# Kernel tuning notes

Hardware: AMD Instinct MI355X
Metric: run time of the kernel (lower is better)

## Reference

```python
import jax, jax.numpy as jnp
import numpy as np

B, V, E = 2, 50000, 400000
FIN, COND, HID, OUT, ENC, EDG = 128, 32, 256, 128, 64, 16
EPS = 1e-5


def setup_inputs() -> dict:
    key = jax.random.key(0)
    ks = jax.random.split(key, 24)
    rn = lambda k, shp, s=0.05: jax.random.normal(k, shp, jnp.float32) * s
    return {
        "x": jax.random.normal(ks[0], (B, V, FIN), jnp.float32),
        "cond_x": jax.random.normal(ks[1], (V, COND), jnp.float32),
        "edge_attr": jax.random.normal(ks[2], (E, EDG), jnp.float32),
        "t": jax.random.normal(ks[3], (B, ENC), jnp.float32),
        "edge_index": jax.random.randint(ks[4], (2, E), 0, V, dtype=jnp.int32),
        # GCNConv weights (in, hid) + bias; Linear weights (hid, out) + bias
        "w_c0": rn(ks[5], (FIN + COND, HID)), "b_c0": rn(ks[6], (HID,)),
        "w_l0": rn(ks[7], (HID, HID)), "b_l0": rn(ks[8], (HID,)),
        "w_c1": rn(ks[9], (HID, HID)), "b_c1": rn(ks[10], (HID,)),
        "w_l1": rn(ks[11], (HID, HID)), "b_l1": rn(ks[12], (HID,)),
        "w_c2": rn(ks[13], (HID, HID)), "b_c2": rn(ks[14], (HID,)),
        "w_l2": rn(ks[15], (HID, OUT)), "b_l2": rn(ks[16], (OUT,)),
        "gn_g": jnp.ones((HID,), jnp.float32), "gn_b": jnp.zeros((HID,), jnp.float32),
        "film_w": rn(ks[17], (ENC, 2 * HID)), "film_b": rn(ks[18], (2 * HID,)),
    }


def _gcn(h, src, dst, dinv, W, b):
    # GCNConv: symmetric-normalized aggregation with self loops, then +bias.
    hw = h @ W  # (B, V, H)
    coef = (dinv[src] * dinv[dst])[None, :, None]            # (1, E, 1)
    self_loop = hw * (dinv * dinv)[None, :, None]            # norm of (i,i) edge
    agg = self_loop.at[:, dst, :].add(hw[:, src, :] * coef)  # scatter-add over dst
    return agg + b


def _groupnorm1(h, gamma, beta):
    # nn.GroupNorm(1, C) applied to (B, C, V): normalize over (C, V) per sample.
    mu = h.mean(axis=(1, 2), keepdims=True)
    var = ((h - mu) ** 2).mean(axis=(1, 2), keepdims=True)
    return (h - mu) * jax.lax.rsqrt(var + EPS) * gamma + beta


def reference(x, cond_x, edge_attr, t, edge_index,
              w_c0, b_c0, w_l0, b_l0, w_c1, b_c1, w_l1, b_l1,
              w_c2, b_c2, w_l2, b_l2, gn_g, gn_b, film_w, film_b):
    src, dst = edge_index[0], edge_index[1]
    deg = jnp.ones((V,), jnp.float32).at[dst].add(1.0)  # 1 = self loop
    dinv = jax.lax.rsqrt(deg)

    x_skip = x
    cond = jnp.broadcast_to(cond_x[None], (x.shape[0], V, COND))
    h = jnp.concatenate([x, cond], axis=-1)  # (B, V, FIN+COND)

    # layer 0: feature dim != hidden -> no norm
    h = jax.nn.relu(_gcn(h, src, dst, dinv, w_c0, b_c0))
    h = jax.nn.relu(h @ w_l0 + b_l0)  # dropout p=0 -> identity

    # layer 1: GroupNorm(1, hidden) then conv/linear
    h = _groupnorm1(h, gn_g, gn_b)
    h = jax.nn.relu(_gcn(h, src, dst, dinv, w_c1, b_c1))
    h = jax.nn.relu(h @ w_l1 + b_l1)

    # final gconv + FiLM + relu + linear + residual
    h = _gcn(h, src, dst, dinv, w_c2, b_c2)
    gb = t @ film_w + film_b                 # (B, 2*HID)
    gamma, beta = gb[:, :HID], gb[:, HID:]
    h = h * gamma[:, None, :] + beta[:, None, :]
    h = jax.nn.relu(h)
    out = h @ w_l2 + b_l2 + x_skip
    return out
```

## Files before the change

### kernel.cpp

```cpp
#include <hip/hip_runtime.h>
#include <stdint.h>

typedef unsigned short u16;
typedef short bf16x8 __attribute__((ext_vector_type(8)));
typedef float f32x4 __attribute__((ext_vector_type(4)));

constexpr int B_ = 2, V_ = 50000, E_ = 400000;
constexpr int FIN_ = 128, COND_ = 32, HID_ = 256, OUT_ = 128, ENC_ = 64;
constexpr int M_ = B_ * V_;
constexpr int MP_ = M_ + 256;
constexpr int K0_ = FIN_ + COND_;
constexpr float EPS_ = 1e-5f;

#define DEV static __device__ __forceinline__

DEV float b2f(u16 u) { union { float f; uint32_t i; } x; x.i = ((uint32_t)u) << 16; return x.f; }
DEV u16 f2b(float f) {
  union { float f; uint32_t i; } x; x.f = f;
  uint32_t r = x.i + 0x7fffu + ((x.i >> 16) & 1u);
  return (u16)(r >> 16);
}
DEV uint32_t pk2(float a, float b) { return (uint32_t)f2b(a) | ((uint32_t)f2b(b) << 16); }

#define GLDS16(gp, lp) __builtin_amdgcn_global_load_lds( \
    (const __attribute__((address_space(1))) void*)(gp), \
    (__attribute__((address_space(3))) void*)(lp), 16, 0, 0)

__global__ void k_count(const int* __restrict__ dst, int* __restrict__ cnt) {
  int e = blockIdx.x * blockDim.x + threadIdx.x;
  if (e < E_) atomicAdd(&cnt[dst[e]], 1);
}

__global__ void k_dinv(const int* __restrict__ cnt, float* __restrict__ dinv) {
  int v = blockIdx.x * blockDim.x + threadIdx.x;
  if (v < V_) dinv[v] = rsqrtf(1.0f + (float)cnt[v]);
}

__global__ __launch_bounds__(1024) void k_scan1(const int* __restrict__ cnt,
                                                int* __restrict__ tmp, int* __restrict__ bsum) {
  __shared__ int s[1024];
  int tid = threadIdx.x;
  int i = blockIdx.x * 1024 + tid;
  int v = (i < V_) ? cnt[i] : 0;
  s[tid] = v;
  __syncthreads();
  for (int off = 1; off < 1024; off <<= 1) {
    int t = (tid >= off) ? s[tid - off] : 0;
    __syncthreads();
    s[tid] += t;
    __syncthreads();
  }
  if (i < V_) tmp[i] = s[tid];
  if (tid == 1023) bsum[blockIdx.x] = s[1023];
}

__global__ void k_scan2(int* __restrict__ bsum, int n) {
  if (threadIdx.x == 0) {
    int a = 0;
    for (int i = 0; i < n; ++i) { a += bsum[i]; bsum[i] = a; }
  }
}

__global__ void k_scan3(const int* __restrict__ cnt, const int* __restrict__ tmp,
                        const int* __restrict__ bsum, int* __restrict__ row_ptr,
                        int* __restrict__ cursor) {
  int i = blockIdx.x * blockDim.x + threadIdx.x;
  if (i >= V_) return;
  int blk = i >> 10;
  int offs = blk ? bsum[blk - 1] : 0;
  int incl = tmp[i] + offs;
  row_ptr[i + 1] = incl;
  cursor[i] = incl - cnt[i];
  if (i == 0) row_ptr[0] = 0;
}

__global__ void k_fill(const int* __restrict__ src, const int* __restrict__ dst,
                       const float* __restrict__ dinv,
                       int* __restrict__ cursor, int2* __restrict__ csr) {
  int e = blockIdx.x * blockDim.x + threadIdx.x;
  if (e < E_) {
    int s = src[e], d = dst[e];
    int p = atomicAdd(&cursor[d], 1);
    float cf = dinv[s] * dinv[d];
    csr[p] = make_int2(s, __float_as_int(cf));
  }
}

__global__ void k_film(const float* __restrict__ t, const float* __restrict__ fw,
                       const float* __restrict__ fb, float* __restrict__ gb) {
  int b = blockIdx.x; int j = threadIdx.x;
  float acc = fb[j];
  for (int k = 0; k < ENC_; ++k) acc += t[b * ENC_ + k] * fw[k * 512 + j];
  gb[b * 512 + j] = acc;
}

__global__ void k_wconv(const float* __restrict__ W, u16* __restrict__ WT, int K, int N) {
  int idx = blockIdx.x * blockDim.x + threadIdx.x;
  if (idx < K * N) {
    int k = idx / N, n = idx % N;
    WT[n * K + k] = f2b(W[idx]);
  }
}

__global__ void k_wconv_g(const float* __restrict__ W, const float* __restrict__ gng,
                          u16* __restrict__ WT, int K, int N) {
  int idx = blockIdx.x * blockDim.x + threadIdx.x;
  if (idx < K * N) {
    int k = idx / N, n = idx % N;
    WT[n * K + k] = f2b(W[idx] * gng[k]);
  }
}

__global__ void k_gnreduce(const float4* __restrict__ part, int nblk,
                           float* __restrict__ stats) {
  int tid = threadIdx.x;
  float s0 = 0.f, ss0 = 0.f, s1 = 0.f, ss1 = 0.f;
  for (int i = tid; i < nblk; i += 256) {
    float4 p = part[i];
    s0 += p.x; ss0 += p.y; s1 += p.z; ss1 += p.w;
  }
  __shared__ float red[4][4];
#pragma unroll
  for (int o = 32; o > 0; o >>= 1) {
    s0  += __shfl_down(s0, o, 64);
    ss0 += __shfl_down(ss0, o, 64);
    s1  += __shfl_down(s1, o, 64);
    ss1 += __shfl_down(ss1, o, 64);
  }
  int w = tid >> 6, ln = tid & 63;
  if (ln == 0) { red[w][0] = s0; red[w][1] = ss0; red[w][2] = s1; red[w][3] = ss1; }
  __syncthreads();
  if (tid == 0) {
    float S0 = red[0][0] + red[1][0] + red[2][0] + red[3][0];
    float SS0 = red[0][1] + red[1][1] + red[2][1] + red[3][1];
    float S1 = red[0][2] + red[1][2] + red[2][2] + red[3][2];
    float SS1 = red[0][3] + red[1][3] + red[2][3] + red[3][3];
    float n = (float)V_ * (float)HID_;
    float mu0 = S0 / n, var0 = SS0 / n - mu0 * mu0;
    float mu1 = S1 / n, var1 = SS1 / n - mu1 * mu1;
    stats[0] = mu0; stats[1] = rsqrtf(var0 + EPS_);
    stats[2] = mu1; stats[3] = rsqrtf(var1 + EPS_);
  }
}

__global__ void k_gnfold(const float* __restrict__ gng, const float* __restrict__ gnb,
                         const float* __restrict__ W, const float* __restrict__ stats,
                         float* __restrict__ kc) {
  int n = blockIdx.x, c = threadIdx.x;
  float wv = W[c * HID_ + n];
  float gw = gng[c] * wv, bw = gnb[c] * wv;
  __shared__ float sg[4], sb[4];
#pragma unroll
  for (int o = 32; o > 0; o >>= 1) {
    gw += __shfl_down(gw, o, 64);
    bw += __shfl_down(bw, o, 64);
  }
  int w = c >> 6, ln = c & 63;
  if (ln == 0) { sg[w] = gw; sb[w] = bw; }
  __syncthreads();
  if (c == 0) {
    float G = sg[0] + sg[1] + sg[2] + sg[3];
    float Bw = sb[0] + sb[1] + sb[2] + sb[3];
    for (int b = 0; b < B_; ++b)
      kc[b * HID_ + n] = Bw - stats[b * 2] * stats[b * 2 + 1] * G;
  }
}

__global__ void k_prep0(const float* __restrict__ x, const float* __restrict__ cond,
                        u16* __restrict__ A0) {
  int idx = blockIdx.x * blockDim.x + threadIdx.x;
  if (idx >= M_ * K0_ / 4) return;
  int e = idx * 4;
  int r = e / K0_, c = e % K0_;
  float4 v;
  if (c < FIN_) v = *(const float4*)&x[(size_t)r * FIN_ + c];
  else { int vv = r % V_; v = *(const float4*)&cond[(size_t)vv * COND_ + (c - FIN_)]; }
  uint2 o;
  o.x = pk2(v.x, v.y);
  o.y = pk2(v.z, v.w);
  *(uint2*)&A0[e] = o;
}

template<int MODE>
__global__ __launch_bounds__(256) void k_gather(
    const u16* __restrict__ hw, const float* __restrict__ dinv,
    const int* __restrict__ row_ptr, const int2* __restrict__ csr,
    const float* __restrict__ bias, const float* __restrict__ gb,
    u16* __restrict__ out)
{
  __shared__ f32x4 redA[3][2][32];
  __shared__ f32x4 redB[3][2][32];
  const int v   = blockIdx.x;
  const int tid = threadIdx.x;
  const int nb  = tid >> 6;
  const int b   = (tid >> 5) & 1;
  const int l   = tid & 31;
  const int c0  = l * 8;

  const float dv = dinv[v];
  const int beg = row_ptr[v], end = row_ptr[v + 1];

  float acc[8];
#pragma unroll
  for (int k = 0; k < 8; ++k) acc[k] = 0.f;

  int j = beg + nb;
  for (; j + 4 < end; j += 8) {
    int2 e0 = csr[j];
    int2 e1 = csr[j + 4];
    float cf0 = __int_as_float(e0.y);
    float cf1 = __int_as_float(e1.y);
    uint4 u0 = *(const uint4*)&hw[((size_t)b * V_ + e0.x) * HID_ + c0];
    uint4 u1 = *(const uint4*)&hw[((size_t)b * V_ + e1.x) * HID_ + c0];
    u16 a0[8]; *(uint4*)a0 = u0;
    u16 a1[8]; *(uint4*)a1 = u1;
#pragma unroll
    for (int k = 0; k < 8; ++k) acc[k] += b2f(a0[k]) * cf0;
#pragma unroll
    for (int k = 0; k < 8; ++k) acc[k] += b2f(a1[k]) * cf1;
  }
  if (j < end) {
    int2 e0 = csr[j];
    float cf0 = __int_as_float(e0.y);
    uint4 u0 = *(const uint4*)&hw[((size_t)b * V_ + e0.x) * HID_ + c0];
    u16 a0[8]; *(uint4*)a0 = u0;
#pragma unroll
    for (int k = 0; k < 8; ++k) acc[k] += b2f(a0[k]) * cf0;
  }

  if (nb > 0) {
    redA[nb - 1][b][l] = f32x4{acc[0], acc[1], acc[2], acc[3]};
    redB[nb - 1][b][l] = f32x4{acc[4], acc[5], acc[6], acc[7]};
  }
  __syncthreads();
  if (nb == 0) {
#pragma unroll
    for (int g = 0; g < 3; ++g) {
      f32x4 ra = redA[g][b][l], rb = redB[g][b][l];
      acc[0] += ra[0]; acc[1] += ra[1]; acc[2] += ra[2]; acc[3] += ra[3];
      acc[4] += rb[0]; acc[5] += rb[1]; acc[6] += rb[2]; acc[7] += rb[3];
    }
    float sl = dv * dv;
    uint4 u = *(const uint4*)&hw[((size_t)b * V_ + v) * HID_ + c0];
    u16 us[8]; *(uint4*)us = u;
#pragma unroll
    for (int k = 0; k < 8; ++k) {
      float a = acc[k] + b2f(us[k]) * sl + bias[c0 + k];
      if (MODE == 1) a = fmaxf(a, 0.f);
      if (MODE == 2) {
        a = a * gb[b * 512 + c0 + k] + gb[b * 512 + 256 + c0 + k];
        a = fmaxf(a, 0.f);
      }
      acc[k] = a;
    }
    uint4 o;
    o.x = pk2(acc[0], acc[1]);
    o.y = pk2(acc[2], acc[3]);
    o.z = pk2(acc[4], acc[5]);
    o.w = pk2(acc[6], acc[7]);
    *(uint4*)&out[((size_t)b * V_ + v) * HID_ + c0] = o;
  }
}

template<int EPI, int K, int N>
__global__ __launch_bounds__(256) void k_gemm_g(
    const u16* __restrict__ A, const u16* __restrict__ WT,
    const float* __restrict__ p0,
    const float* __restrict__ stats,
    const float* __restrict__ xres,
    float4* __restrict__ part,
    void* __restrict__ Out)
{
  constexpr int BM = 128, BN = 128, BK = 32;
  __shared__ alignas(16) u16 As[BM * BK];
  __shared__ alignas(16) u16 Bs[BN * BK];
  __shared__ float sred[4][4];
  const int tile_m = blockIdx.x * BM;
  const int n0 = blockIdx.y * BN;
  const int tid = threadIdx.x;
  const int wave = tid >> 6, lane = tid & 63;
  const int wm = (wave >> 1) * 64, wn = (wave & 1) * 64;
  const int lr = lane & 15, lkg = lane >> 4;
  const int phys = lkg ^ ((lr >> 1) & 3);

  f32x4 acc[4][4];
#pragma unroll
  for (int i = 0; i < 4; ++i)
#pragma unroll
    for (int jj = 0; jj < 4; ++jj) acc[i][jj] = {0.f, 0.f, 0.f, 0.f};

  for (int kb = 0; kb < K; kb += BK) {
#pragma unroll
    for (int it = 0; it < 2; ++it) {
      int c = tid + it * 256;
      int row = c >> 2;
      int sslot = (c & 3) ^ ((row >> 1) & 3);
      GLDS16(A + (size_t)(tile_m + row) * K + kb + sslot * 8,
             &As[(it * 256 + wave * 64) * 8]);
    }
#pragma unroll
    for (int it = 0; it < 2; ++it) {
      int c = tid + it * 256;
      int row = c >> 2;
      int sslot = (c & 3) ^ ((row >> 1) & 3);
      GLDS16(WT + (size_t)(n0 + row) * K + kb + sslot * 8,
             &Bs[(it * 256 + wave * 64) * 8]);
    }
    __syncthreads();
    bf16x8 af[4], bf[4];
#pragma unroll
    for (int fm = 0; fm < 4; ++fm) af[fm] = *(const bf16x8*)&As[(wm + fm * 16 + lr) * BK + phys * 8];
#pragma unroll
    for (int fn = 0; fn < 4; ++fn) bf[fn] = *(const bf16x8*)&Bs[(wn + fn * 16 + lr) * BK + phys * 8];
#pragma unroll
    for (int fm = 0; fm < 4; ++fm)
#pragma unroll
      for (int fn = 0; fn < 4; ++fn)
        acc[fm][fn] = __builtin_amdgcn_mfma_f32_16x16x32_bf16(bf[fn], af[fm], acc[fm][fn], 0, 0, 0);
    __syncthreads();
  }

  float s0 = 0.f, ss0 = 0.f, s1 = 0.f, ss1 = 0.f;
#pragma unroll
  for (int fm = 0; fm < 4; ++fm) {
    const int row = tile_m + wm + fm * 16 + lr;
    if (row >= M_) continue;
#pragma unroll
    for (int fn = 0; fn < 4; ++fn) {
      const int colb = n0 + wn + fn * 16 + lkg * 4;
      float v0 = acc[fm][fn][0], v1 = acc[fm][fn][1];
      float v2 = acc[fm][fn][2], v3 = acc[fm][fn][3];
      if (EPI == 1 || EPI == 4) {
        float4 bs = *(const float4*)&p0[colb];
        v0 = fmaxf(v0 + bs.x, 0.f); v1 = fmaxf(v1 + bs.y, 0.f);
        v2 = fmaxf(v2 + bs.z, 0.f); v3 = fmaxf(v3 + bs.w, 0.f);
      }
      if (EPI == 4) {
        if (row >= V_) { s1 += v0 + v1 + v2 + v3; ss1 += v0*v0 + v1*v1 + v2*v2 + v3*v3; }
        else           { s0 += v0 + v1 + v2 + v3; ss0 += v0*v0 + v1*v1 + v2*v2 + v3*v3; }
      }
      if (EPI == 3) {
        int bb = (row >= V_) ? 1 : 0;
        float rs = stats[bb * 2 + 1];
        float4 kcv = *(const float4*)&p0[bb * N + colb];
        v0 = v0 * rs + kcv.x; v1 = v1 * rs + kcv.y;
        v2 = v2 * rs + kcv.z; v3 = v3 * rs + kcv.w;
      }
      if (EPI == 2) {
        float4 bs = *(const float4*)&p0[colb];
        float4 xr = *(const float4*)&xres[(size_t)row * N + colb];
        float4 o;
        o.x = v0 + bs.x + xr.x; o.y = v1 + bs.y + xr.y;
        o.z = v2 + bs.z + xr.z; o.w = v3 + bs.w + xr.w;
        *(float4*)&((float*)Out)[(size_t)row * N + colb] = o;
      } else {
        uint2 o;
        o.x = pk2(v0, v1);
        o.y = pk2(v2, v3);
        *(uint2*)&((u16*)Out)[(size_t)row * N + colb] = o;
      }
    }
  }
  if (EPI == 4) {
#pragma unroll
    for (int o = 32; o > 0; o >>= 1) {
      s0  += __shfl_down(s0, o, 64);
      ss0 += __shfl_down(ss0, o, 64);
      s1  += __shfl_down(s1, o, 64);
      ss1 += __shfl_down(ss1, o, 64);
    }
    if (lane == 0) { sred[wave][0] = s0; sred[wave][1] = ss0; sred[wave][2] = s1; sred[wave][3] = ss1; }
    __syncthreads();
    if (tid == 0) {
      float4 p;
      p.x = sred[0][0] + sred[1][0] + sred[2][0] + sred[3][0];
      p.y = sred[0][1] + sred[1][1] + sred[2][1] + sred[3][1];
      p.z = sred[0][2] + sred[1][2] + sred[2][2] + sred[3][2];
      p.w = sred[0][3] + sred[1][3] + sred[2][3] + sred[3][3];
      part[blockIdx.y * gridDim.x + blockIdx.x] = p;
    }
  }
}

extern "C" void kernel_launch(void* const* d_in, const int* in_sizes, int n_in,
                              void* d_out, int out_size, void* d_ws, size_t ws_size,
                              hipStream_t stream) {
  (void)in_sizes; (void)n_in; (void)out_size; (void)ws_size;
  const float* x      = (const float*)d_in[0];
  const float* cond_x = (const float*)d_in[1];
  const float* t      = (const float*)d_in[3];
  const int*   ei     = (const int*)d_in[4];
  const float* w_c0 = (const float*)d_in[5];  const float* b_c0 = (const float*)d_in[6];
  const float* w_l0 = (const float*)d_in[7];  const float* b_l0 = (const float*)d_in[8];
  const float* w_c1 = (const float*)d_in[9];  const float* b_c1 = (const float*)d_in[10];
  const float* w_l1 = (const float*)d_in[11]; const float* b_l1 = (const float*)d_in[12];
  const float* w_c2 = (const float*)d_in[13]; const float* b_c2 = (const float*)d_in[14];
  const float* w_l2 = (const float*)d_in[15]; const float* b_l2 = (const float*)d_in[16];
  const float* gn_g = (const float*)d_in[17]; const float* gn_b = (const float*)d_in[18];
  const float* film_w = (const float*)d_in[19]; const float* film_b = (const float*)d_in[20];

  char* wsp = (char*)d_ws;
  size_t off = 0;
  auto alloc = [&](size_t bytes) -> char* {
    char* p = wsp + off; off += (bytes + 255) & ~(size_t)255; return p;
  };
  constexpr int GM = (M_ + 127) / 128;
  int*   cnt       = (int*)  alloc((size_t)V_ * 4);
  int*   row_ptr   = (int*)  alloc((size_t)(V_ + 1) * 4);
  int*   cursor    = (int*)  alloc((size_t)V_ * 4);
  int2*  csr       = (int2*) alloc((size_t)E_ * 8);
  int*   scan_tmp  = (int*)  alloc((size_t)V_ * 4);
  int*   scan_bsum = (int*)  alloc(64 * 4);
  float* dinv      = (float*)alloc((size_t)V_ * 4);
  float* stats     = (float*)alloc(16);
  float4* part     = (float4*)alloc((size_t)GM * 2 * 16);
  float* gb        = (float*)alloc(2 * 512 * 4);
  float* kc        = (float*)alloc(2 * HID_ * 4);
  u16* wc0T  = (u16*)alloc((size_t)256 * 160 * 2);
  u16* wl0T  = (u16*)alloc((size_t)256 * 256 * 2);
  u16* wc1Tg = (u16*)alloc((size_t)256 * 256 * 2);
  u16* wl1T  = (u16*)alloc((size_t)256 * 256 * 2);
  u16* wc2T  = (u16*)alloc((size_t)256 * 256 * 2);
  u16* wl2T  = (u16*)alloc((size_t)128 * 256 * 2);
  u16* A0    = (u16*)alloc((size_t)MP_ * K0_ * 2);
  u16* HW    = (u16*)alloc((size_t)MP_ * HID_ * 2);
  u16* HA    = (u16*)alloc((size_t)MP_ * HID_ * 2);
  u16* HB    = (u16*)alloc((size_t)MP_ * HID_ * 2);

  const int* srcI = ei;
  const int* dstI = ei + E_;

  hipMemsetAsync(cnt, 0, (size_t)V_ * 4, stream);

  constexpr int NBLK = (V_ + 1023) / 1024;
  k_count<<<dim3((E_ + 255) / 256), dim3(256), 0, stream>>>(dstI, cnt);
  k_dinv <<<dim3((V_ + 255) / 256), dim3(256), 0, stream>>>(cnt, dinv);
  k_scan1<<<dim3(NBLK), dim3(1024), 0, stream>>>(cnt, scan_tmp, scan_bsum);
  k_scan2<<<dim3(1), dim3(64), 0, stream>>>(scan_bsum, NBLK);
  k_scan3<<<dim3((V_ + 255) / 256), dim3(256), 0, stream>>>(cnt, scan_tmp, scan_bsum, row_ptr, cursor);
  k_fill <<<dim3((E_ + 255) / 256), dim3(256), 0, stream>>>(srcI, dstI, dinv, cursor, csr);
  k_film <<<dim3(2), dim3(512), 0, stream>>>(t, film_w, film_b, gb);

  k_wconv  <<<dim3((160 * 256 + 255) / 256), dim3(256), 0, stream>>>(w_c0, wc0T, 160, 256);
  k_wconv  <<<dim3((256 * 256 + 255) / 256), dim3(256), 0, stream>>>(w_l0, wl0T, 256, 256);
  k_wconv_g<<<dim3((256 * 256 + 255) / 256), dim3(256), 0, stream>>>(w_c1, gn_g, wc1Tg, 256, 256);
  k_wconv  <<<dim3((256 * 256 + 255) / 256), dim3(256), 0, stream>>>(w_l1, wl1T, 256, 256);
  k_wconv  <<<dim3((256 * 256 + 255) / 256), dim3(256), 0, stream>>>(w_c2, wc2T, 256, 256);
  k_wconv  <<<dim3((256 * 128 + 255) / 256), dim3(256), 0, stream>>>(w_l2, wl2T, 256, 128);

  k_prep0<<<dim3(M_ * K0_ / 4 / 256), dim3(256), 0, stream>>>(x, cond_x, A0);

  k_gemm_g<0, 160, 256><<<dim3(GM, 2), 256, 0, stream>>>(A0, wc0T, nullptr, nullptr, nullptr, nullptr, HW);
  k_gather<1><<<dim3(V_), 256, 0, stream>>>(HW, dinv, row_ptr, csr, b_c0, nullptr, HA);
  k_gemm_g<4, 256, 256><<<dim3(GM, 2), 256, 0, stream>>>(HA, wl0T, b_l0, nullptr, nullptr, part, HB);

  k_gnreduce<<<dim3(1), dim3(256), 0, stream>>>(part, GM * 2, stats);
  k_gnfold <<<dim3(256), dim3(256), 0, stream>>>(gn_g, gn_b, w_c1, stats, kc);

  k_gemm_g<3, 256, 256><<<dim3(GM, 2), 256, 0, stream>>>(HB, wc1Tg, kc, stats, nullptr, nullptr, HW);
  k_gather<1><<<dim3(V_), 256, 0, stream>>>(HW, dinv, row_ptr, csr, b_c1, nullptr, HA);
  k_gemm_g<1, 256, 256><<<dim3(GM, 2), 256, 0, stream>>>(HA, wl1T, b_l1, nullptr, nullptr, nullptr, HB);

  k_gemm_g<0, 256, 256><<<dim3(GM, 2), 256, 0, stream>>>(HB, wc2T, nullptr, nullptr, nullptr, nullptr, HW);
  k_gather<2><<<dim3(V_), 256, 0, stream>>>(HW, dinv, row_ptr, csr, b_c2, gb, HA);
  k_gemm_g<2, 256, 128><<<dim3(GM, 1), 256, 0, stream>>>(HA, wl2T, b_l2, nullptr, x, nullptr, (void*)d_out);
}
```

Measured before the change: 525.2 us.

## Aggregate before GEMM and fuse each conv GEMM with following linear GEMM

Reorders each GCN layer to aggregate over neighbours first (A·H then W), so layer 0 gathers the 160-wide input instead of the 256-wide projection. Each conv GEMM is then fused with the following linear GEMM in one kernel that keeps the 64x256 intermediate tile in LDS, which removes one full write and read of the hidden activations per layer. The GroupNorm fold is moved after aggregation by using a per-node rowsum of edge coefficients. In exchange the fused kernel uses smaller 64-row tiles and needs a large LDS footprint, which may lower occupancy, and the gather kernel idles some lanes when the width is 160.

```diff
diff --git a/kernel.cpp b/kernel.cpp
--- a/kernel.cpp
+++ b/kernel.cpp
@@ -84,6 +84,17 @@
     float cf = dinv[s] * dinv[d];
     csr[p] = make_int2(s, __float_as_int(cf));
   }
+}
+
+__global__ void k_rowsum(const float* __restrict__ dinv, const int* __restrict__ row_ptr,
+                         const int2* __restrict__ csr, float* __restrict__ rowsum) {
+  int v = blockIdx.x * blockDim.x + threadIdx.x;
+  if (v >= V_) return;
+  float dv = dinv[v];
+  float s = dv * dv;
+  int e = row_ptr[v + 1];
+  for (int j = row_ptr[v]; j < e; ++j) s += __int_as_float(csr[j].y);
+  rowsum[v] = s;
 }
 
 __global__ void k_film(const float* __restrict__ t, const float* __restrict__ fw,
@@ -181,11 +192,10 @@
   *(uint2*)&A0[e] = o;
 }
 
-template<int MODE>
+template<int KW>
 __global__ __launch_bounds__(256) void k_gather(
     const u16* __restrict__ hw, const float* __restrict__ dinv,
     const int* __restrict__ row_ptr, const int2* __restrict__ csr,
-    const float* __restrict__ bias, const float* __restrict__ gb,
     u16* __restrict__ out)
 {
   __shared__ f32x4 redA[3][2][32];
@@ -196,6 +206,7 @@
   const int b   = (tid >> 5) & 1;
   const int l   = tid & 31;
   const int c0  = l * 8;
+  const bool act = l < (KW / 8);
 
   const float dv = dinv[v];
   const int beg = row_ptr[v], end = row_ptr[v + 1];
@@ -204,28 +215,30 @@
 #pragma unroll
   for (int k = 0; k < 8; ++k) acc[k] = 0.f;
 
-  int j = beg + nb;
-  for (; j + 4 < end; j += 8) {
-    int2 e0 = csr[j];
-    int2 e1 = csr[j + 4];
-    float cf0 = __int_as_float(e0.y);
-    float cf1 = __int_as_float(e1.y);
-    uint4 u0 = *(const uint4*)&hw[((size_t)b * V_ + e0.x) * HID_ + c0];
-    uint4 u1 = *(const uint4*)&hw[((size_t)b * V_ + e1.x) * HID_ + c0];
-    u16 a0[8]; *(uint4*)a0 = u0;
-    u16 a1[8]; *(uint4*)a1 = u1;
-#pragma unroll
-    for (int k = 0; k < 8; ++k) acc[k] += b2f(a0[k]) * cf0;
-#pragma unroll
-    for (int k = 0; k < 8; ++k) acc[k] += b2f(a1[k]) * cf1;
-  }
-  if (j < end) {
-    int2 e0 = csr[j];
-    float cf0 = __int_as_float(e0.y);
-    uint4 u0 = *(const uint4*)&hw[((size_t)b * V_ + e0.x) * HID_ + c0];
-    u16 a0[8]; *(uint4*)a0 = u0;
-#pragma unroll
-    for (int k = 0; k < 8; ++k) acc[k] += b2f(a0[k]) * cf0;
+  if (act) {
+    int j = beg + nb;
+    for (; j + 4 < end; j += 8) {
+      int2 e0 = csr[j];
+      int2 e1 = csr[j + 4];
+      float cf0 = __int_as_float(e0.y);
+      float cf1 = __int_as_float(e1.y);
+      uint4 u0 = *(const uint4*)&hw[((size_t)b * V_ + e0.x) * KW + c0];
+      uint4 u1 = *(const uint4*)&hw[((size_t)b * V_ + e1.x) * KW + c0];
+      u16 a0[8]; *(uint4*)a0 = u0;
+      u16 a1[8]; *(uint4*)a1 = u1;
+#pragma unroll
+      for (int k = 0; k < 8; ++k) acc[k] += b2f(a0[k]) * cf0;
+#pragma unroll
+      for (int k = 0; k < 8; ++k) acc[k] += b2f(a1[k]) * cf1;
+    }
+    if (j < end) {
+      int2 e0 = csr[j];
+      float cf0 = __int_as_float(e0.y);
+      uint4 u0 = *(const uint4*)&hw[((size_t)b * V_ + e0.x) * KW + c0];
+      u16 a0[8]; *(uint4*)a0 = u0;
+#pragma unroll
+      for (int k = 0; k < 8; ++k) acc[k] += b2f(a0[k]) * cf0;
+    }
   }
 
   if (nb > 0) {
@@ -233,7 +246,7 @@
     redB[nb - 1][b][l] = f32x4{acc[4], acc[5], acc[6], acc[7]};
   }
   __syncthreads();
-  if (nb == 0) {
+  if (nb == 0 && act) {
 #pragma unroll
     for (int g = 0; g < 3; ++g) {
       f32x4 ra = redA[g][b][l], rb = redB[g][b][l];
@@ -241,45 +254,37 @@
       acc[4] += rb[0]; acc[5] += rb[1]; acc[6] += rb[2]; acc[7] += rb[3];
     }
     float sl = dv * dv;
-    uint4 u = *(const uint4*)&hw[((size_t)b * V_ + v) * HID_ + c0];
+    uint4 u = *(const uint4*)&hw[((size_t)b * V_ + v) * KW + c0];
     u16 us[8]; *(uint4*)us = u;
 #pragma unroll
-    for (int k = 0; k < 8; ++k) {
-      float a = acc[k] + b2f(us[k]) * sl + bias[c0 + k];
-      if (MODE == 1) a = fmaxf(a, 0.f);
-      if (MODE == 2) {
-        a = a * gb[b * 512 + c0 + k] + gb[b * 512 + 256 + c0 + k];
-        a = fmaxf(a, 0.f);
-      }
-      acc[k] = a;
-    }
+    for (int k = 0; k < 8; ++k) acc[k] += b2f(us[k]) * sl;
     uint4 o;
     o.x = pk2(acc[0], acc[1]);
     o.y = pk2(acc[2], acc[3]);
     o.z = pk2(acc[4], acc[5]);
     o.w = pk2(acc[6], acc[7]);
-    *(uint4*)&out[((size_t)b * V_ + v) * HID_ + c0] = o;
-  }
-}
-
-template<int EPI, int K, int N>
-__global__ __launch_bounds__(256) void k_gemm_g(
-    const u16* __restrict__ A, const u16* __restrict__ WT,
-    const float* __restrict__ p0,
-    const float* __restrict__ stats,
-    const float* __restrict__ xres,
-    float4* __restrict__ part,
+    *(uint4*)&out[((size_t)b * V_ + v) * KW + c0] = o;
+  }
+}
+
+template<int P1E, int P2E, int K1, int N2>
+__global__ __launch_bounds__(256) void k_pair(
+    const u16* __restrict__ A, const u16* __restrict__ W1T, const u16* __restrict__ W2T,
+    const float* __restrict__ b1, const float* __restrict__ b2,
+    const float* __restrict__ stats, const float* __restrict__ kc,
+    const float* __restrict__ rowsum, const float* __restrict__ gb,
+    const float* __restrict__ xres, float4* __restrict__ part,
     void* __restrict__ Out)
 {
-  constexpr int BM = 128, BN = 128, BK = 32;
-  __shared__ alignas(16) u16 As[BM * BK];
-  __shared__ alignas(16) u16 Bs[BN * BK];
+  constexpr int BM = 64, BK = 32, N1 = 256;
+  constexpr int FN2 = N2 / 64;
+  __shared__ alignas(16) u16 Asg[BM * BK];
+  __shared__ alignas(16) u16 Bsg[N1 * BK];
+  __shared__ alignas(16) u16 T1[BM * N1];
   __shared__ float sred[4][4];
   const int tile_m = blockIdx.x * BM;
-  const int n0 = blockIdx.y * BN;
   const int tid = threadIdx.x;
   const int wave = tid >> 6, lane = tid & 63;
-  const int wm = (wave >> 1) * 64, wn = (wave & 1) * 64;
   const int lr = lane & 15, lkg = lane >> 4;
   const int phys = lkg ^ ((lr >> 1) & 3);
 
@@ -287,81 +292,141 @@
 #pragma unroll
   for (int i = 0; i < 4; ++i)
 #pragma unroll
-    for (int jj = 0; jj < 4; ++jj) acc[i][jj] = {0.f, 0.f, 0.f, 0.f};
-
-  for (int kb = 0; kb < K; kb += BK) {
-#pragma unroll
-    for (int it = 0; it < 2; ++it) {
+    for (int j = 0; j < 4; ++j) acc[i][j] = {0.f, 0.f, 0.f, 0.f};
+
+  for (int kb = 0; kb < K1; kb += BK) {
+    {
+      int row = tid >> 2;
+      int sslot = (tid & 3) ^ ((row >> 1) & 3);
+      GLDS16(A + (size_t)(tile_m + row) * K1 + kb + sslot * 8, &Asg[(wave * 64) * 8]);
+    }
+#pragma unroll
+    for (int it = 0; it < 4; ++it) {
       int c = tid + it * 256;
       int row = c >> 2;
       int sslot = (c & 3) ^ ((row >> 1) & 3);
-      GLDS16(A + (size_t)(tile_m + row) * K + kb + sslot * 8,
-             &As[(it * 256 + wave * 64) * 8]);
-    }
-#pragma unroll
-    for (int it = 0; it < 2; ++it) {
+      GLDS16(W1T + (size_t)row * K1 + kb + sslot * 8, &Bsg[(it * 256 + wave * 64) * 8]);
+    }
+    __syncthreads();
+    bf16x8 af[4], bf[4];
+#pragma unroll
+    for (int fm = 0; fm < 4; ++fm) af[fm] = *(const bf16x8*)&Asg[(fm * 16 + lr) * BK + phys * 8];
+#pragma unroll
+    for (int fn = 0; fn < 4; ++fn) bf[fn] = *(const bf16x8*)&Bsg[(wave * 64 + fn * 16 + lr) * BK + phys * 8];
+#pragma unroll
+    for (int fm = 0; fm < 4; ++fm)
+#pragma unroll
+      for (int fn = 0; fn < 4; ++fn)
+        acc[fm][fn] = __builtin_amdgcn_mfma_f32_16x16x32_bf16(bf[fn], af[fm], acc[fm][fn], 0, 0, 0);
+    __syncthreads();
+  }
+
+#pragma unroll
+  for (int fm = 0; fm < 4; ++fm) {
+    const int row = fm * 16 + lr;
+    const int gr = tile_m + row;
+    const int bb = (gr >= V_) ? 1 : 0;
+    float rsc = 1.f, rsum = 0.f;
+    if (P1E == 1) {
+      rsc = stats[bb * 2 + 1];
+      int node = (gr < M_) ? (gr - bb * V_) : 0;
+      rsum = rowsum[node];
+    }
+#pragma unroll
+    for (int fn = 0; fn < 4; ++fn) {
+      const int colb = wave * 64 + fn * 16 + lkg * 4;
+      float v0 = acc[fm][fn][0], v1 = acc[fm][fn][1];
+      float v2 = acc[fm][fn][2], v3 = acc[fm][fn][3];
+      float4 bs = *(const float4*)&b1[colb];
+      if (P1E == 0) {
+        v0 = fmaxf(v0 + bs.x, 0.f); v1 = fmaxf(v1 + bs.y, 0.f);
+        v2 = fmaxf(v2 + bs.z, 0.f); v3 = fmaxf(v3 + bs.w, 0.f);
+      }
+      if (P1E == 1) {
+        float4 kcv = *(const float4*)&kc[bb * 256 + colb];
+        v0 = fmaxf(v0 * rsc + rsum * kcv.x + bs.x, 0.f);
+        v1 = fmaxf(v1 * rsc + rsum * kcv.y + bs.y, 0.f);
+        v2 = fmaxf(v2 * rsc + rsum * kcv.z + bs.z, 0.f);
+        v3 = fmaxf(v3 * rsc + rsum * kcv.w + bs.w, 0.f);
+      }
+      if (P1E == 2) {
+        float4 g = *(const float4*)&gb[bb * 512 + colb];
+        float4 be = *(const float4*)&gb[bb * 512 + 256 + colb];
+        v0 = fmaxf((v0 + bs.x) * g.x + be.x, 0.f);
+        v1 = fmaxf((v1 + bs.y) * g.y + be.y, 0.f);
+        v2 = fmaxf((v2 + bs.z) * g.z + be.z, 0.f);
+        v3 = fmaxf((v3 + bs.w) * g.w + be.w, 0.f);
+      }
+      int pg = (colb >> 2) ^ ((row & 7) << 1);
+      uint2 o; o.x = pk2(v0, v1); o.y = pk2(v2, v3);
+      *(uint2*)&T1[row * 256 + pg * 4] = o;
+    }
+  }
+  __syncthreads();
+
+  f32x4 acc2[4][FN2];
+#pragma unroll
+  for (int i = 0; i < 4; ++i)
+#pragma unroll
+    for (int j = 0; j < FN2; ++j) acc2[i][j] = {0.f, 0.f, 0.f, 0.f};
+
+  for (int kb2 = 0; kb2 < 256; kb2 += BK) {
+#pragma unroll
+    for (int it = 0; it < FN2; ++it) {
       int c = tid + it * 256;
       int row = c >> 2;
       int sslot = (c & 3) ^ ((row >> 1) & 3);
-      GLDS16(WT + (size_t)(n0 + row) * K + kb + sslot * 8,
-             &Bs[(it * 256 + wave * 64) * 8]);
-    }
-    __syncthreads();
-    bf16x8 af[4], bf[4];
-#pragma unroll
-    for (int fm = 0; fm < 4; ++fm) af[fm] = *(const bf16x8*)&As[(wm + fm * 16 + lr) * BK + phys * 8];
-#pragma unroll
-    for (int fn = 0; fn < 4; ++fn) bf[fn] = *(const bf16x8*)&Bs[(wn + fn * 16 + lr) * BK + phys * 8];
+      GLDS16(W2T + (size_t)row * 256 + kb2 + sslot * 8, &Bsg[(it * 256 + wave * 64) * 8]);
+    }
+    __syncthreads();
+    bf16x8 af2[4], bf2[FN2];
+#pragma unroll
+    for (int fm = 0; fm < 4; ++fm) {
+      int row = fm * 16 + lr;
+      int pg = ((kb2 >> 2) + lkg * 2) ^ ((row & 7) << 1);
+      af2[fm] = *(const bf16x8*)&T1[row * 256 + pg * 4];
+    }
+#pragma unroll
+    for (int fn = 0; fn < FN2; ++fn)
+      bf2[fn] = *(const bf16x8*)&Bsg[(wave * (N2 / 4) + fn * 16 + lr) * BK + phys * 8];
 #pragma unroll
     for (int fm = 0; fm < 4; ++fm)
 #pragma unroll
-      for (int fn = 0; fn < 4; ++fn)
-        acc[fm][fn] = __builtin_amdgcn_mfma_f32_16x16x32_bf16(bf[fn], af[fm], acc[fm][fn], 0, 0, 0);
+      for (int fn = 0; fn < FN2; ++fn)
+        acc2[fm][fn] = __builtin_amdgcn_mfma_f32_16x16x32_bf16(bf2[fn], af2[fm], acc2[fm][fn], 0, 0, 0);
     __syncthreads();
   }
 
   float s0 = 0.f, ss0 = 0.f, s1 = 0.f, ss1 = 0.f;
 #pragma unroll
   for (int fm = 0; fm < 4; ++fm) {
-    const int row = tile_m + wm + fm * 16 + lr;
+    const int row = tile_m + fm * 16 + lr;
     if (row >= M_) continue;
 #pragma unroll
-    for (int fn = 0; fn < 4; ++fn) {
-      const int colb = n0 + wn + fn * 16 + lkg * 4;
-      float v0 = acc[fm][fn][0], v1 = acc[fm][fn][1];
-      float v2 = acc[fm][fn][2], v3 = acc[fm][fn][3];
-      if (EPI == 1 || EPI == 4) {
-        float4 bs = *(const float4*)&p0[colb];
+    for (int fn = 0; fn < FN2; ++fn) {
+      const int colb = wave * (N2 / 4) + fn * 16 + lkg * 4;
+      float v0 = acc2[fm][fn][0], v1 = acc2[fm][fn][1];
+      float v2 = acc2[fm][fn][2], v3 = acc2[fm][fn][3];
+      float4 bs = *(const float4*)&b2[colb];
+      if (P2E == 0 || P2E == 1) {
         v0 = fmaxf(v0 + bs.x, 0.f); v1 = fmaxf(v1 + bs.y, 0.f);
         v2 = fmaxf(v2 + bs.z, 0.f); v3 = fmaxf(v3 + bs.w, 0.f);
-      }
-      if (EPI == 4) {
-        if (row >= V_) { s1 += v0 + v1 + v2 + v3; ss1 += v0*v0 + v1*v1 + v2*v2 + v3*v3; }
-        else           { s0 += v0 + v1 + v2 + v3; ss0 += v0*v0 + v1*v1 + v2*v2 + v3*v3; }
-      }
-      if (EPI == 3) {
-        int bb = (row >= V_) ? 1 : 0;
-        float rs = stats[bb * 2 + 1];
-        float4 kcv = *(const float4*)&p0[bb * N + colb];
-        v0 = v0 * rs + kcv.x; v1 = v1 * rs + kcv.y;
-        v2 = v2 * rs + kcv.z; v3 = v3 * rs + kcv.w;
-      }
-      if (EPI == 2) {
-        float4 bs = *(const float4*)&p0[colb];
-        float4 xr = *(const float4*)&xres[(size_t)row * N + colb];
+        if (P2E == 1) {
+          if (row >= V_) { s1 += v0 + v1 + v2 + v3; ss1 += v0*v0 + v1*v1 + v2*v2 + v3*v3; }
+          else           { s0 += v0 + v1 + v2 + v3; ss0 += v0*v0 + v1*v1 + v2*v2 + v3*v3; }
+        }
+        uint2 o; o.x = pk2(v0, v1); o.y = pk2(v2, v3);
+        *(uint2*)&((u16*)Out)[(size_t)row * N2 + colb] = o;
+      } else {
+        float4 xr = *(const float4*)&xres[(size_t)row * N2 + colb];
         float4 o;
         o.x = v0 + bs.x + xr.x; o.y = v1 + bs.y + xr.y;
         o.z = v2 + bs.z + xr.z; o.w = v3 + bs.w + xr.w;
-        *(float4*)&((float*)Out)[(size_t)row * N + colb] = o;
-      } else {
-        uint2 o;
-        o.x = pk2(v0, v1);
-        o.y = pk2(v2, v3);
-        *(uint2*)&((u16*)Out)[(size_t)row * N + colb] = o;
+        *(float4*)&((float*)Out)[(size_t)row * N2 + colb] = o;
       }
     }
   }
-  if (EPI == 4) {
+  if (P2E == 1) {
 #pragma unroll
     for (int o = 32; o > 0; o >>= 1) {
       s0  += __shfl_down(s0, o, 64);
@@ -377,7 +442,7 @@
       p.y = sred[0][1] + sred[1][1] + sred[2][1] + sred[3][1];
       p.z = sred[0][2] + sred[1][2] + sred[2][2] + sred[3][2];
       p.w = sred[0][3] + sred[1][3] + sred[2][3] + sred[3][3];
-      part[blockIdx.y * gridDim.x + blockIdx.x] = p;
+      part[blockIdx.x] = p;
     }
   }
 }
@@ -404,7 +469,7 @@
   auto alloc = [&](size_t bytes) -> char* {
     char* p = wsp + off; off += (bytes + 255) & ~(size_t)255; return p;
   };
-  constexpr int GM = (M_ + 127) / 128;
+  constexpr int GM64 = (M_ + 63) / 64;
   int*   cnt       = (int*)  alloc((size_t)V_ * 4);
   int*   row_ptr   = (int*)  alloc((size_t)(V_ + 1) * 4);
   int*   cursor    = (int*)  alloc((size_t)V_ * 4);
@@ -412,8 +477,9 @@
   int*   scan_tmp  = (int*)  alloc((size_t)V_ * 4);
   int*   scan_bsum = (int*)  alloc(64 * 4);
   float* dinv      = (float*)alloc((size_t)V_ * 4);
+  float* rowsum    = (float*)alloc((size_t)V_ * 4);
   float* stats     = (float*)alloc(16);
-  float4* part     = (float4*)alloc((size_t)GM * 2 * 16);
+  float4* part     = (float4*)alloc((size_t)GM64 * 16);
   float* gb        = (float*)alloc(2 * 512 * 4);
   float* kc        = (float*)alloc(2 * HID_ * 4);
   u16* wc0T  = (u16*)alloc((size_t)256 * 160 * 2);
@@ -423,9 +489,9 @@
   u16* wc2T  = (u16*)alloc((size_t)256 * 256 * 2);
   u16* wl2T  = (u16*)alloc((size_t)128 * 256 * 2);
   u16* A0    = (u16*)alloc((size_t)MP_ * K0_ * 2);
-  u16* HW    = (u16*)alloc((size_t)MP_ * HID_ * 2);
-  u16* HA    = (u16*)alloc((size_t)MP_ * HID_ * 2);
+  u16* HA0   = (u16*)alloc((size_t)MP_ * K0_ * 2);
   u16* HB    = (u16*)alloc((size_t)MP_ * HID_ * 2);
+  u16* HA1   = (u16*)alloc((size_t)MP_ * HID_ * 2);
 
   const int* srcI = ei;
   const int* dstI = ei + E_;
@@ -439,6 +505,7 @@
   k_scan2<<<dim3(1), dim3(64), 0, stream>>>(scan_bsum, NBLK);
   k_scan3<<<dim3((V_ + 255) / 256), dim3(256), 0, stream>>>(cnt, scan_tmp, scan_bsum, row_ptr, cursor);
   k_fill <<<dim3((E_ + 255) / 256), dim3(256), 0, stream>>>(srcI, dstI, dinv, cursor, csr);
+  k_rowsum<<<dim3((V_ + 255) / 256), dim3(256), 0, stream>>>(dinv, row_ptr, csr, rowsum);
   k_film <<<dim3(2), dim3(512), 0, stream>>>(t, film_w, film_b, gb);
 
   k_wconv  <<<dim3((160 * 256 + 255) / 256), dim3(256), 0, stream>>>(w_c0, wc0T, 160, 256);
@@ -450,18 +517,18 @@
 
   k_prep0<<<dim3(M_ * K0_ / 4 / 256), dim3(256), 0, stream>>>(x, cond_x, A0);
 
-  k_gemm_g<0, 160, 256><<<dim3(GM, 2), 256, 0, stream>>>(A0, wc0T, nullptr, nullptr, nullptr, nullptr, HW);
-  k_gather<1><<<dim3(V_), 256, 0, stream>>>(HW, dinv, row_ptr, csr, b_c0, nullptr, HA);
-  k_gemm_g<4, 256, 256><<<dim3(GM, 2), 256, 0, stream>>>(HA, wl0T, b_l0, nullptr, nullptr, part, HB);
-
-  k_gnreduce<<<dim3(1), dim3(256), 0, stream>>>(part, GM * 2, stats);
+  k_gather<160><<<dim3(V_), 256, 0, stream>>>(A0, dinv, row_ptr, csr, HA0);
+  k_pair<0, 1, 160, 256><<<dim3(GM64), 256, 0, stream>>>(
+      HA0, wc0T, wl0T, b_c0, b_l0, nullptr, nullptr, nullptr, nullptr, nullptr, part, HB);
+
+  k_gnreduce<<<dim3(1), dim3(256), 0, stream>>>(part, GM64, stats);
   k_gnfold <<<dim3(256), dim3(256), 0, stream>>>(gn_g, gn_b, w_c1, stats, kc);
 
-  k_gemm_g<3, 256, 256><<<dim3(GM, 2), 256, 0, stream>>>(HB, wc1Tg, kc, stats, nullptr, nullptr, HW);
-  k_gather<1><<<dim3(V_), 256, 0, stream>>>(HW, dinv, row_ptr, csr, b_c1, nullptr, HA);
-  k_gemm_g<1, 256, 256><<<dim3(GM, 2), 256, 0, stream>>>(HA, wl1T, b_l1, nullptr, nullptr, nullptr, HB);
-
-  k_gemm_g<0, 256, 256><<<dim3(GM, 2), 256, 0, stream>>>(HB, wc2T, nullptr, nullptr, nullptr, nullptr, HW);
-  k_gather<2><<<dim3(V_), 256, 0, stream>>>(HW, dinv, row_ptr, csr, b_c2, gb, HA);
-  k_gemm_g<2, 256, 128><<<dim3(GM, 1), 256, 0, stream>>>(HA, wl2T, b_l2, nullptr, x, nullptr, (void*)d_out);
-}
+  k_gather<256><<<dim3(V_), 256, 0, stream>>>(HB, dinv, row_ptr, csr, HA1);
+  k_pair<1, 0, 256, 256><<<dim3(GM64), 256, 0, stream>>>(
+      HA1, wc1Tg, wl1T, b_c1, b_l1, stats, kc, rowsum, nullptr, nullptr, nullptr, HB);
+
+  k_gather<256><<<dim3(V_), 256, 0, stream>>>(HB, dinv, row_ptr, csr, HA1);
+  k_pair<2, 2, 256, 128><<<dim3(GM64), 256, 0, stream>>>(
+      HA1, wc2T, wl2T, b_c2, b_l2, nullptr, nullptr, nullptr, gb, x, nullptr, (void*)d_out);
+}
```

New measurement: 515.5 us. No clear change (-1.9%).
